# Kernel tuning notes

Hardware: AMD Instinct MI355X
Metric: run time of the kernel (lower is better)

Reference implementation:

```python
import jax, jax.numpy as jnp
import numpy as np

N_USERS = 100000
N_ITEMS = 100000
N_BICLIQUES = 50000
NNZ = 2000000
D = 64


def setup_inputs() -> dict:
    key = jax.random.key(0)
    k1, k2, k3, k4, k5, k6 = jax.random.split(key, 6)
    return {
        "user_emb": jax.random.normal(k1, (N_USERS, D), dtype=jnp.float32),
        "item_emb": jax.random.normal(k2, (N_ITEMS, D), dtype=jnp.float32),
        "hv_rows": jax.random.randint(k3, (NNZ,), 0, N_BICLIQUES, dtype=jnp.int32),
        "hv_cols": jax.random.randint(k4, (NNZ,), 0, N_ITEMS, dtype=jnp.int32),
        "hv_vals": jnp.ones((NNZ,), dtype=jnp.float32),
        "hu_rows": jax.random.randint(k5, (NNZ,), 0, N_USERS, dtype=jnp.int32),
        "hu_cols": jax.random.randint(k6, (NNZ,), 0, N_BICLIQUES, dtype=jnp.int32),
        "hu_vals": jnp.ones((NNZ,), dtype=jnp.float32),
        "n_bicliques": N_BICLIQUES,
        "n_users": N_USERS,
    }


def _spmm_mean(rows, cols, vals, dense, num_segments):
    # out[r] = (sum_{e: rows[e]==r} vals[e] * dense[cols[e]]) / max(degree[r], treat 0 as 1)
    # degree[r] = sum of vals on row r (matches torch.sparse.sum(dim=1)).
    num = jax.ops.segment_sum(vals[:, None] * dense[cols], rows, num_segments=num_segments)
    deg = jax.ops.segment_sum(vals, rows, num_segments=num_segments)
    deg = jnp.where(deg == 0, 1.0, deg)[:, None]
    return num / deg


def reference(user_emb, item_emb, hv_rows, hv_cols, hv_vals, hu_rows, hu_cols, hu_vals, n_bicliques, n_users):
    # Hop 1: biclique features = row-mean of item embeddings via H_v [n_bicliques, n_items]
    biclique_features = _spmm_mean(hv_rows, hv_cols, hv_vals, item_emb, n_bicliques)
    # Hop 2: user local view = row-mean of biclique features via H_u [n_users, n_bicliques]
    user_local_view = _spmm_mean(hu_rows, hu_cols, hu_vals, biclique_features, n_users)
    return user_local_view
```

## Files before the change

### kernel.cpp

```cpp
#include <hip/hip_runtime.h>
#include <hip/hip_fp16.h>


#define DIM 64
#define CAP 5888
#define CHUNK 8192
#define P1B 512
#define EPT (CHUNK / P1B)
#define NB1 391
#define NB2 391

__global__ __launch_bounds__(P1B) void pass1_bin_kernel(
    const int* __restrict__ rows1, const int* __restrict__ cols1,
    const float* __restrict__ vals1, int nnz1, int nc1,
    const int* __restrict__ rows2, const int* __restrict__ cols2,
    const float* __restrict__ vals2, int nnz2,
    int* __restrict__ bincnt1, int2* __restrict__ st1,
    int* __restrict__ bincnt2, int2* __restrict__ st2) {
    __shared__ int hist[400];
    __shared__ int cur[400];
    const int* rows; const int* cols; const float* vals;
    int nnz, shift, nb, chunk_id;
    int* bincnt; int2* st;
    if ((int)blockIdx.x < nc1) {
        rows = rows1; cols = cols1; vals = vals1; nnz = nnz1;
        shift = 7; nb = NB1; chunk_id = blockIdx.x; bincnt = bincnt1; st = st1;
    } else {
        rows = rows2; cols = cols2; vals = vals2; nnz = nnz2;
        shift = 8; nb = NB2; chunk_id = blockIdx.x - nc1; bincnt = bincnt2; st = st2;
    }
    int t = threadIdx.x;
    for (int i = t; i < nb; i += P1B) hist[i] = 0;
    __syncthreads();
    int begin = chunk_id * CHUNK;

    int r[EPT]; int c[EPT]; float v[EPT];
    #pragma unroll
    for (int k = 0; k < EPT; ++k) {
        int idx = begin + k * P1B + t;
        bool ok = idx < nnz;
        r[k] = ok ? rows[idx] : -1;
        c[k] = ok ? cols[idx] : 0;
        v[k] = ok ? vals[idx] : 0.0f;
        if (ok) atomicAdd(&hist[r[k] >> shift], 1);
    }
    __syncthreads();
    for (int i = t; i < nb; i += P1B) {
        int h = hist[i];
        if (h > 0) cur[i] = i * CAP + atomicAdd(&bincnt[i], h);
    }
    __syncthreads();
    #pragma unroll
    for (int k = 0; k < EPT; ++k) {
        if (r[k] >= 0) {
            int b = r[k] >> shift;
            int pos = atomicAdd(&cur[b], 1);
            int key = ((r[k] - (b << shift)) << 17) | c[k];
            st[pos] = make_int2(key, __float_as_int(v[k]));
        }
    }
}

__global__ void f32_to_f16_kernel(const float4* __restrict__ in,
                                  int2* __restrict__ outp, int n4) {
    int i = blockIdx.x * blockDim.x + threadIdx.x;
    if (i >= n4) return;
    float4 x = in[i];
    __half2 h0 = __float22half2_rn(make_float2(x.x, x.y));
    __half2 h1 = __float22half2_rn(make_float2(x.z, x.w));
    int2 pk;
    pk.x = *(int*)&h0;
    pk.y = *(int*)&h1;
    outp[i] = pk;
}

template <int RPB, bool DST_HALF>
__global__ __launch_bounds__(1024, 8) void sort_gather_kernel(
    const int2* __restrict__ st, const int* __restrict__ bincnt,
    const __half* __restrict__ src,
    void* __restrict__ dstv,
    int n_rows) {
    __shared__ int2 edges[CAP];
    __shared__ int excl[RPB];
    __shared__ int cur[RPB];
    int b = blockIdx.x;
    int t = threadIdx.x;
    int row0 = b * RPB;
    int cnt_b = bincnt[b];
    const int2* bst = st + (size_t)b * CAP;

    if (t < RPB) cur[t] = 0;
    __syncthreads();
    for (int i = t; i < cnt_b; i += 1024)
        atomicAdd(&cur[bst[i].x >> 17], 1);
    __syncthreads();
    if (t < RPB) excl[t] = cur[t];
    __syncthreads();
    for (int off = 1; off < RPB; off <<= 1) {
        int vv = 0;
        if (t < RPB && t >= off) vv = excl[t - off];
        __syncthreads();
        if (t < RPB) excl[t] += vv;
        __syncthreads();
    }
    if (t < RPB) {
        int e = excl[t] - cur[t];
        excl[t] = e;
        cur[t] = e;
    }
    __syncthreads();
    for (int i = t; i < cnt_b; i += 1024) {
        int2 kv = bst[i];
        int pos = atomicAdd(&cur[kv.x >> 17], 1);
        edges[pos] = make_int2(kv.x & 0x1FFFF, kv.y);
    }
    __syncthreads();
    int wave = t >> 6;
    int lane = t & 63;
    int sub = lane >> 4;
    int ld  = lane & 15;
    for (int rl = wave; rl < RPB; rl += 16) {
        int row = row0 + rl;
        if (row >= n_rows) break;
        int start = excl[rl];
        int end   = cur[rl];
        float ax = 0.f, ay = 0.f, az = 0.f, aw = 0.f, vsum = 0.f;
        for (int i = start; i < end; i += 8) {
            int i0 = i + sub, i1 = i + sub + 4;
            int c0 = 0, c1 = 0; float v0 = 0.f, v1 = 0.f;
            if (i0 < end) { int2 e = edges[i0]; c0 = e.x; v0 = __int_as_float(e.y); }
            if (i1 < end) { int2 e = edges[i1]; c1 = e.x; v1 = __int_as_float(e.y); }
            int2 r0 = *(const int2*)(src + (long long)c0 * DIM + ld * 4);
            int2 r1 = *(const int2*)(src + (long long)c1 * DIM + ld * 4);
            float2 a0 = __half22float2(*(__half2*)&r0.x);
            float2 b0 = __half22float2(*(__half2*)&r0.y);
            float2 a1 = __half22float2(*(__half2*)&r1.x);
            float2 b1 = __half22float2(*(__half2*)&r1.y);
            ax += v0 * a0.x + v1 * a1.x;
            ay += v0 * a0.y + v1 * a1.y;
            az += v0 * b0.x + v1 * b1.x;
            aw += v0 * b0.y + v1 * b1.y;
            vsum += v0 + v1;
        }
        #pragma unroll
        for (int off = 16; off <= 32; off <<= 1) {
            ax += __shfl_xor(ax, off);
            ay += __shfl_xor(ay, off);
            az += __shfl_xor(az, off);
            aw += __shfl_xor(aw, off);
            vsum += __shfl_xor(vsum, off);
        }
        float d = (vsum == 0.0f) ? 1.0f : vsum;
        if (sub == 0) {
            float inv = 1.0f / d;
            if (DST_HALF) {
                __half* dst = (__half*)dstv;
                __half2 o0 = __float22half2_rn(make_float2(ax * inv, ay * inv));
                __half2 o1 = __float22half2_rn(make_float2(az * inv, aw * inv));
                int2 pk;
                pk.x = *(int*)&o0;
                pk.y = *(int*)&o1;
                *(int2*)(dst + (long long)row * DIM + ld * 4) = pk;
            } else {
                float* dst = (float*)dstv;
                float4 o = make_float4(ax * inv, ay * inv, az * inv, aw * inv);
                *(float4*)(dst + (long long)row * DIM + ld * 4) = o;
            }
        }
    }
}

extern "C" void kernel_launch(void* const* d_in, const int* in_sizes, int n_in,
                              void* d_out, int out_size, void* d_ws, size_t ws_size,
                              hipStream_t stream) {
    const float* item_emb = (const float*)d_in[1];
    const int*   hv_rows  = (const int*)d_in[2];
    const int*   hv_cols  = (const int*)d_in[3];
    const float* hv_vals  = (const float*)d_in[4];
    const int*   hu_rows  = (const int*)d_in[5];
    const int*   hu_cols  = (const int*)d_in[6];
    const float* hu_vals  = (const float*)d_in[7];

    const int nnz1 = in_sizes[2];
    const int nnz2 = in_sizes[5];
    const int n_items = in_sizes[1] / DIM;
    const int n_b  = 50000;
    const int n_u  = out_size / DIM;

    float* out = (float*)d_out;

    char* p = (char*)d_ws;
    __half* item_h  = (__half*)p; p += (size_t)n_items * DIM * sizeof(__half);
    __half* bf_h    = (__half*)p; p += (size_t)n_b * DIM * sizeof(__half);
    int*   bincnt1 = (int*)p;   p += 400 * sizeof(int);
    int*   bincnt2 = (int*)p;   p += 400 * sizeof(int);
    int2*  st1     = (int2*)p;  p += (size_t)NB1 * CAP * sizeof(int2);
    int2*  st2     = (int2*)p;  p += (size_t)NB2 * CAP * sizeof(int2);

    hipMemsetAsync(bincnt1, 0, 800 * sizeof(int), stream);

    int n4 = n_items * DIM / 4;
    f32_to_f16_kernel<<<(n4 + 255) / 256, 256, 0, stream>>>(
        (const float4*)item_emb, (int2*)item_h, n4);

    int nc1 = (nnz1 + CHUNK - 1) / CHUNK;
    int nc2 = (nnz2 + CHUNK - 1) / CHUNK;
    pass1_bin_kernel<<<nc1 + nc2, P1B, 0, stream>>>(
        hv_rows, hv_cols, hv_vals, nnz1, nc1,
        hu_rows, hu_cols, hu_vals, nnz2,
        bincnt1, st1, bincnt2, st2);

    sort_gather_kernel<128, true><<<NB1, 1024, 0, stream>>>(
        st1, bincnt1, item_h, bf_h, n_b);
    sort_gather_kernel<256, false><<<NB2, 1024, 0, stream>>>(
        st2, bincnt2, bf_h, out, n_u);
}
```

Baseline: 253.6 us.

## Halve bin size, use smaller blocks, and unroll gather to four edges

Each bin now covers half as many rows (64/128 instead of 128/256), so there are about twice as many gather blocks, each with 512 threads and half the shared-memory edge buffer. This should raise occupancy and spread the irregular gather across more CUs. The inner gather loop now handles four edges per sub-lane per iteration instead of two, giving more loads in flight. The bin count is clamped to CAP, so a bin that overflows would silently drop edges. Address math was also shortened to 32-bit arithmetic.

```diff
diff --git a/kernel.cpp b/kernel.cpp
--- a/kernel.cpp
+++ b/kernel.cpp
@@ -3,12 +3,10 @@
 
 
 #define DIM 64
-#define CAP 5888
+#define CAP 2944
 #define CHUNK 8192
 #define P1B 512
 #define EPT (CHUNK / P1B)
-#define NB1 391
-#define NB2 391
 
 __global__ __launch_bounds__(P1B) void pass1_bin_kernel(
     const int* __restrict__ rows1, const int* __restrict__ cols1,
@@ -17,17 +15,17 @@
     const float* __restrict__ vals2, int nnz2,
     int* __restrict__ bincnt1, int2* __restrict__ st1,
     int* __restrict__ bincnt2, int2* __restrict__ st2) {
-    __shared__ int hist[400];
-    __shared__ int cur[400];
+    __shared__ int hist[800];
+    __shared__ int cur[800];
     const int* rows; const int* cols; const float* vals;
     int nnz, shift, nb, chunk_id;
     int* bincnt; int2* st;
     if ((int)blockIdx.x < nc1) {
         rows = rows1; cols = cols1; vals = vals1; nnz = nnz1;
-        shift = 7; nb = NB1; chunk_id = blockIdx.x; bincnt = bincnt1; st = st1;
+        shift = 6; nb = 800; chunk_id = blockIdx.x; bincnt = bincnt1; st = st1;
     } else {
         rows = rows2; cols = cols2; vals = vals2; nnz = nnz2;
-        shift = 8; nb = NB2; chunk_id = blockIdx.x - nc1; bincnt = bincnt2; st = st2;
+        shift = 7; nb = 800; chunk_id = blockIdx.x - nc1; bincnt = bincnt2; st = st2;
     }
     int t = threadIdx.x;
     for (int i = t; i < nb; i += P1B) hist[i] = 0;
@@ -75,7 +73,7 @@
 }
 
 template <int RPB, bool DST_HALF>
-__global__ __launch_bounds__(1024, 8) void sort_gather_kernel(
+__global__ __launch_bounds__(512, 8) void sort_gather_kernel(
     const int2* __restrict__ st, const int* __restrict__ bincnt,
     const __half* __restrict__ src,
     void* __restrict__ dstv,
@@ -83,15 +81,15 @@
     __shared__ int2 edges[CAP];
     __shared__ int excl[RPB];
     __shared__ int cur[RPB];
-    int b = blockIdx.x;
-    int t = threadIdx.x;
-    int row0 = b * RPB;
-    int cnt_b = bincnt[b];
+    const int b = blockIdx.x;
+    const int t = threadIdx.x;
+    const int row0 = b * RPB;
+    int cnt_b = min(bincnt[b], CAP);
     const int2* bst = st + (size_t)b * CAP;
 
     if (t < RPB) cur[t] = 0;
     __syncthreads();
-    for (int i = t; i < cnt_b; i += 1024)
+    for (int i = t; i < cnt_b; i += 512)
         atomicAdd(&cur[bst[i].x >> 17], 1);
     __syncthreads();
     if (t < RPB) excl[t] = cur[t];
@@ -109,38 +107,56 @@
         cur[t] = e;
     }
     __syncthreads();
-    for (int i = t; i < cnt_b; i += 1024) {
+    for (int i = t; i < cnt_b; i += 512) {
         int2 kv = bst[i];
         int pos = atomicAdd(&cur[kv.x >> 17], 1);
         edges[pos] = make_int2(kv.x & 0x1FFFF, kv.y);
     }
     __syncthreads();
-    int wave = t >> 6;
-    int lane = t & 63;
-    int sub = lane >> 4;
-    int ld  = lane & 15;
-    for (int rl = wave; rl < RPB; rl += 16) {
+
+    const int wave = t >> 6;
+    const int lane = t & 63;
+    const int sub = lane >> 4;
+    const int ld  = lane & 15;
+    const __half* srcl = src + ld * 4;
+    for (int rl = wave; rl < RPB; rl += 8) {
         int row = row0 + rl;
         if (row >= n_rows) break;
         int start = excl[rl];
         int end   = cur[rl];
         float ax = 0.f, ay = 0.f, az = 0.f, aw = 0.f, vsum = 0.f;
-        for (int i = start; i < end; i += 8) {
-            int i0 = i + sub, i1 = i + sub + 4;
-            int c0 = 0, c1 = 0; float v0 = 0.f, v1 = 0.f;
-            if (i0 < end) { int2 e = edges[i0]; c0 = e.x; v0 = __int_as_float(e.y); }
-            if (i1 < end) { int2 e = edges[i1]; c1 = e.x; v1 = __int_as_float(e.y); }
-            int2 r0 = *(const int2*)(src + (long long)c0 * DIM + ld * 4);
-            int2 r1 = *(const int2*)(src + (long long)c1 * DIM + ld * 4);
+        for (int i = start + sub; i < end; i += 16) {
+            int i1 = i + 4, i2 = i + 8, i3 = i + 12;
+            float v0 = 0.f, v1 = 0.f, v2 = 0.f, v3 = 0.f;
+            int2 r0 = make_int2(0, 0), r1 = r0, r2 = r0, r3 = r0;
+            {   int2 e = edges[i];
+                v0 = __int_as_float(e.y);
+                r0 = *(const int2*)(srcl + (e.x << 6)); }
+            if (i1 < end) {
+                int2 e = edges[i1];
+                v1 = __int_as_float(e.y);
+                r1 = *(const int2*)(srcl + (e.x << 6)); }
+            if (i2 < end) {
+                int2 e = edges[i2];
+                v2 = __int_as_float(e.y);
+                r2 = *(const int2*)(srcl + (e.x << 6)); }
+            if (i3 < end) {
+                int2 e = edges[i3];
+                v3 = __int_as_float(e.y);
+                r3 = *(const int2*)(srcl + (e.x << 6)); }
             float2 a0 = __half22float2(*(__half2*)&r0.x);
             float2 b0 = __half22float2(*(__half2*)&r0.y);
             float2 a1 = __half22float2(*(__half2*)&r1.x);
             float2 b1 = __half22float2(*(__half2*)&r1.y);
-            ax += v0 * a0.x + v1 * a1.x;
-            ay += v0 * a0.y + v1 * a1.y;
-            az += v0 * b0.x + v1 * b1.x;
-            aw += v0 * b0.y + v1 * b1.y;
-            vsum += v0 + v1;
+            float2 a2 = __half22float2(*(__half2*)&r2.x);
+            float2 b2 = __half22float2(*(__half2*)&r2.y);
+            float2 a3 = __half22float2(*(__half2*)&r3.x);
+            float2 b3 = __half22float2(*(__half2*)&r3.y);
+            ax += v0 * a0.x + v1 * a1.x + v2 * a2.x + v3 * a3.x;
+            ay += v0 * a0.y + v1 * a1.y + v2 * a2.y + v3 * a3.y;
+            az += v0 * b0.x + v1 * b1.x + v2 * b2.x + v3 * b3.x;
+            aw += v0 * b0.y + v1 * b1.y + v2 * b2.y + v3 * b3.y;
+            vsum += (v0 + v1) + (v2 + v3);
         }
         #pragma unroll
         for (int off = 16; off <= 32; off <<= 1) {
@@ -160,11 +176,11 @@
                 int2 pk;
                 pk.x = *(int*)&o0;
                 pk.y = *(int*)&o1;
-                *(int2*)(dst + (long long)row * DIM + ld * 4) = pk;
+                *(int2*)(dst + row * DIM + ld * 4) = pk;
             } else {
                 float* dst = (float*)dstv;
                 float4 o = make_float4(ax * inv, ay * inv, az * inv, aw * inv);
-                *(float4*)(dst + (long long)row * DIM + ld * 4) = o;
+                *(float4*)(dst + row * DIM + ld * 4) = o;
             }
         }
     }
@@ -187,17 +203,20 @@
     const int n_b  = 50000;
     const int n_u  = out_size / DIM;
 
+    const int nb1 = (n_b + 63) >> 6;
+    const int nb2 = (n_u + 127) >> 7;
+
     float* out = (float*)d_out;
 
     char* p = (char*)d_ws;
     __half* item_h  = (__half*)p; p += (size_t)n_items * DIM * sizeof(__half);
     __half* bf_h    = (__half*)p; p += (size_t)n_b * DIM * sizeof(__half);
-    int*   bincnt1 = (int*)p;   p += 400 * sizeof(int);
-    int*   bincnt2 = (int*)p;   p += 400 * sizeof(int);
-    int2*  st1     = (int2*)p;  p += (size_t)NB1 * CAP * sizeof(int2);
-    int2*  st2     = (int2*)p;  p += (size_t)NB2 * CAP * sizeof(int2);
-
-    hipMemsetAsync(bincnt1, 0, 800 * sizeof(int), stream);
+    int*   bincnt1 = (int*)p;   p += 800 * sizeof(int);
+    int*   bincnt2 = (int*)p;   p += 800 * sizeof(int);
+    int2*  st1     = (int2*)p;  p += (size_t)nb1 * CAP * sizeof(int2);
+    int2*  st2     = (int2*)p;  p += (size_t)nb2 * CAP * sizeof(int2);
+
+    hipMemsetAsync(bincnt1, 0, 1600 * sizeof(int), stream);
 
     int n4 = n_items * DIM / 4;
     f32_to_f16_kernel<<<(n4 + 255) / 256, 256, 0, stream>>>(
@@ -210,8 +229,8 @@
         hu_rows, hu_cols, hu_vals, nnz2,
         bincnt1, st1, bincnt2, st2);
 
-    sort_gather_kernel<128, true><<<NB1, 1024, 0, stream>>>(
+    sort_gather_kernel<64, true><<<nb1, 512, 0, stream>>>(
         st1, bincnt1, item_h, bf_h, n_b);
-    sort_gather_kernel<256, false><<<NB2, 1024, 0, stream>>>(
+    sort_gather_kernel<128, false><<<nb2, 512, 0, stream>>>(
         st2, bincnt2, bf_h, out, n_u);
 }
```

After: 255.4 us. Within noise of the previous version (+0.7%).
